# Optimization experiments

Measured on AMD Instinct MI355X. Metric: run time of the kernel, lower is better.

The kernel has to match this reference:

```python
import jax, jax.numpy as jnp
import numpy as np

E = 3_200_000
D = 16
N = 100_000


def setup_inputs() -> dict:
    key = jax.random.key(0)
    k1, k2 = jax.random.split(key)
    x = jax.random.normal(k1, (E, D), dtype=jnp.float32)
    edge_dst = jax.random.randint(k2, (E,), 0, N, dtype=jnp.int64)
    return {"x": x, "edge_dst": edge_dst, "num_nodes": N}


def reference(x, edge_dst, num_nodes):
    # sum_over_neighbours: scatter-add edge features to destination atoms -> [N, D]
    summed = jax.ops.segment_sum(x, edge_dst, num_segments=num_nodes)
    # number_of_neighbours(include_central_atom=True): per-atom edge count + 1
    counts = jax.ops.segment_sum(
        jnp.ones((x.shape[0],), dtype=x.dtype), edge_dst, num_segments=num_nodes
    ) + jnp.asarray(1.0, dtype=x.dtype)
    # left_aligned_div by sqrt(counts): broadcast counts over trailing feature dims
    return summed / jnp.sqrt(counts)[:, None]
```

## Files before the change

### kernel.cpp

```cpp
#include <hip/hip_runtime.h>

#define DFEAT 16
#define NPB 64
#define NPB_SHIFT 6
#define EB 8192
#define EB_SHIFT 13
#define BIN_THREADS 1024
#define SCAN_BLOCKS 256
#define SCAN_THREADS 256
#define SORT_CAP 4096

__global__ void na_bin_kernel(const int* __restrict__ edge_dst,
                              unsigned short* __restrict__ rank,
                              int* __restrict__ hist,
                              int E, int B, int nblocks) {
    extern __shared__ int h[];
    const int b = blockIdx.x;
    const int t = threadIdx.x;
    for (int i = t; i < B; i += BIN_THREADS) h[i] = 0;
    __syncthreads();
    const int base = b * EB;
    #pragma unroll
    for (int j = 0; j < EB / BIN_THREADS; ++j) {
        int e = base + j * BIN_THREADS + t;
        if (e < E) {
            int k = edge_dst[e] >> NPB_SHIFT;
            int r = atomicAdd(&h[k], 1);
            rank[e] = (unsigned short)r;
        }
    }
    __syncthreads();
    for (int i = t; i < B; i += BIN_THREADS)
        hist[(size_t)i * nblocks + b] = h[i];
}

__global__ void na_scan_partials(const int* __restrict__ data,
                                 int* __restrict__ blockSums, int M) {
    __shared__ int lds[SCAN_THREADS];
    const int b = blockIdx.x, t = threadIdx.x;
    const int chb = (M + SCAN_BLOCKS - 1) / SCAN_BLOCKS;
    const int bbeg = b * chb;
    const int bend = min(bbeg + chb, M);
    const int cht = (chb + SCAN_THREADS - 1) / SCAN_THREADS;
    const int beg = min(bbeg + t * cht, bend);
    const int end = min(beg + cht, bend);
    int s = 0;
    for (int i = beg; i < end; ++i) s += data[i];
    lds[t] = s;
    __syncthreads();
    for (int off = SCAN_THREADS / 2; off > 0; off >>= 1) {
        if (t < off) lds[t] += lds[t + off];
        __syncthreads();
    }
    if (t == 0) blockSums[b] = lds[0];
}

__global__ void na_scan_blocksums(const int* __restrict__ blockSums,
                                  int* __restrict__ blockOffs) {
    __shared__ int lds[SCAN_BLOCKS];
    const int t = threadIdx.x;
    int v = blockSums[t];
    lds[t] = v;
    __syncthreads();
    for (int off = 1; off < SCAN_BLOCKS; off <<= 1) {
        int add = (t >= off) ? lds[t - off] : 0;
        __syncthreads();
        lds[t] += add;
        __syncthreads();
    }
    blockOffs[t] = lds[t] - v;
}

__global__ void na_scan_final(int* __restrict__ data,
                              const int* __restrict__ blockOffs, int M) {
    __shared__ int lds[SCAN_THREADS];
    const int b = blockIdx.x, t = threadIdx.x;
    const int chb = (M + SCAN_BLOCKS - 1) / SCAN_BLOCKS;
    const int bbeg = b * chb;
    const int bend = min(bbeg + chb, M);
    const int cht = (chb + SCAN_THREADS - 1) / SCAN_THREADS;
    const int beg = min(bbeg + t * cht, bend);
    const int end = min(beg + cht, bend);
    int s = 0;
    for (int i = beg; i < end; ++i) s += data[i];
    lds[t] = s;
    __syncthreads();
    for (int off = 1; off < SCAN_THREADS; off <<= 1) {
        int add = (t >= off) ? lds[t - off] : 0;
        __syncthreads();
        lds[t] += add;
        __syncthreads();
    }
    int run = blockOffs[b] + lds[t] - s;
    for (int i = beg; i < end; ++i) {
        int c = data[i];
        data[i] = run;
        run += c;
    }
}

__global__ void na_scatter_bin(const int* __restrict__ edge_dst,
                               const unsigned short* __restrict__ rank,
                               const int* __restrict__ offs,
                               int* __restrict__ binned,
                               int E, int nblocks) {
    int e = blockIdx.x * blockDim.x + threadIdx.x;
    if (e >= E) return;
    int n = edge_dst[e];
    int k = n >> NPB_SHIFT;
    int b = e >> EB_SHIFT;
    int pos = offs[(size_t)k * nblocks + b] + (int)rank[e];
    binned[pos] = ((n & (NPB - 1)) << 22) | e;
}

__global__ void na_bucket_sort(int* __restrict__ binned,
                               const int* __restrict__ offs,
                               int* __restrict__ offsets,
                               int E, int N, int B, int nblocks) {
    __shared__ int buf[SORT_CAP];
    __shared__ int cnt[NPB];
    __shared__ int cur[NPB];
    __shared__ int excl[NPB + 1];
    const int k = blockIdx.x;
    const int t = threadIdx.x;

    const int beg = offs[(size_t)k * nblocks];
    const int end = (k + 1 < B) ? offs[(size_t)(k + 1) * nblocks] : E;
    const int sz = end - beg;

    if (t < NPB) { cnt[t] = 0; cur[t] = 0; }
    __syncthreads();

    for (int j = t; j < sz; j += 256) {
        int v = binned[beg + j];
        buf[j] = v;
        atomicAdd(&cnt[v >> 22], 1);
    }
    __syncthreads();

    if (t == 0) {
        int run = 0;
        for (int d = 0; d < NPB; ++d) { excl[d] = run; run += cnt[d]; }
        excl[NPB] = run;
    }
    __syncthreads();

    if (t < NPB) {
        int g = k * NPB + t;
        if (g < N) offsets[g] = beg + excl[t];
    }
    if (k == B - 1 && t == 0) offsets[N] = E;

    for (int j = t; j < sz; j += 256) {
        int v = buf[j];
        int d = v >> 22;
        int r = atomicAdd(&cur[d], 1);
        binned[beg + excl[d] + r] = v & 0x3FFFFF;
    }
}

__global__ void na_gather_kernel(const float* __restrict__ x,
                                 const int* __restrict__ edge_list,
                                 const int* __restrict__ offsets,
                                 float* __restrict__ out,
                                 int N) {
    int tid = blockIdx.x * blockDim.x + threadIdx.x;
    int node = tid >> 4;
    int f = tid & 15;
    if (node >= N) return;

    int beg = offsets[node];
    int end = offsets[node + 1];

    float acc = 0.0f;
    int i = beg;
    for (; i + 8 <= end; i += 8) {
        int e0 = edge_list[i + 0], e1 = edge_list[i + 1];
        int e2 = edge_list[i + 2], e3 = edge_list[i + 3];
        int e4 = edge_list[i + 4], e5 = edge_list[i + 5];
        int e6 = edge_list[i + 6], e7 = edge_list[i + 7];
        float v0 = x[(size_t)e0 * DFEAT + f];
        float v1 = x[(size_t)e1 * DFEAT + f];
        float v2 = x[(size_t)e2 * DFEAT + f];
        float v3 = x[(size_t)e3 * DFEAT + f];
        float v4 = x[(size_t)e4 * DFEAT + f];
        float v5 = x[(size_t)e5 * DFEAT + f];
        float v6 = x[(size_t)e6 * DFEAT + f];
        float v7 = x[(size_t)e7 * DFEAT + f];
        acc += ((v0 + v1) + (v2 + v3)) + ((v4 + v5) + (v6 + v7));
    }
    for (; i < end; ++i) acc += x[(size_t)edge_list[i] * DFEAT + f];

    float scale = rsqrtf((float)(end - beg) + 1.0f);
    out[(size_t)node * DFEAT + f] = acc * scale;
}

extern "C" void kernel_launch(void* const* d_in, const int* in_sizes, int n_in,
                              void* d_out, int out_size, void* d_ws, size_t ws_size,
                              hipStream_t stream) {
    const float* x        = (const float*)d_in[0];
    const int*   edge_dst = (const int*)d_in[1];
    float*       out      = (float*)d_out;

    const int E = in_sizes[1];
    const int N = out_size / DFEAT;
    const int B = (N + NPB - 1) >> NPB_SHIFT;
    const int nblocks = (E + EB - 1) >> EB_SHIFT;
    const int M = B * nblocks;

    unsigned short* rank = (unsigned short*)d_ws;
    int* binned    = (int*)((char*)d_ws + (((size_t)E * 2 + 3) & ~(size_t)3));
    int* hist      = binned + E;
    int* offsets   = hist + M;
    int* blockSums = offsets + N + 1;
    int* blockOffs = blockSums + SCAN_BLOCKS;

    na_bin_kernel<<<nblocks, BIN_THREADS, B * sizeof(int), stream>>>(
        edge_dst, rank, hist, E, B, nblocks);
    na_scan_partials<<<SCAN_BLOCKS, SCAN_THREADS, 0, stream>>>(hist, blockSums, M);
    na_scan_blocksums<<<1, SCAN_BLOCKS, 0, stream>>>(blockSums, blockOffs);
    na_scan_final<<<SCAN_BLOCKS, SCAN_THREADS, 0, stream>>>(hist, blockOffs, M);
    na_scatter_bin<<<(E + 255) / 256, 256, 0, stream>>>(
        edge_dst, rank, hist, binned, E, nblocks);
    na_bucket_sort<<<B, 256, 0, stream>>>(binned, hist, offsets, E, N, B, nblocks);

    const int gthreads = N * 16;
    na_gather_kernel<<<(gthreads + 255) / 256, 256, 0, stream>>>(
        x, binned, offsets, out, N);
}
```

Before: 141.9 us.

## Fuse bucket sort with gather, keep sorted edges in LDS, use float4 loads

The per-bucket local sort and the per-node gather are merged into one kernel. Sorted edge indices stay in shared memory instead of being written back to global memory and re-read, and the separate offsets array is dropped. The gather now reads x as float4, with four edge-strided lanes per node combined by shuffles. This removes one launch and one round trip of the edge list through global memory. In exchange the doubled shared-memory footprint may lower occupancy, and a slow fallback path handles buckets larger than the sort capacity.

```diff
diff --git a/kernel.cpp b/kernel.cpp
--- a/kernel.cpp
+++ b/kernel.cpp
@@ -113,14 +113,18 @@
     binned[pos] = ((n & (NPB - 1)) << 22) | e;
 }
 
-__global__ void na_bucket_sort(int* __restrict__ binned,
-                               const int* __restrict__ offs,
-                               int* __restrict__ offsets,
-                               int E, int N, int B, int nblocks) {
+__global__ __launch_bounds__(256, 4)
+void na_sort_gather(const float* __restrict__ x,
+                    const int* __restrict__ binned,
+                    const int* __restrict__ offs,
+                    float* __restrict__ out,
+                    int E, int N, int B, int nblocks) {
     __shared__ int buf[SORT_CAP];
+    __shared__ int sorted[SORT_CAP];
     __shared__ int cnt[NPB];
     __shared__ int cur[NPB];
     __shared__ int excl[NPB + 1];
+
     const int k = blockIdx.x;
     const int t = threadIdx.x;
 
@@ -131,68 +135,89 @@
     if (t < NPB) { cnt[t] = 0; cur[t] = 0; }
     __syncthreads();
 
-    for (int j = t; j < sz; j += 256) {
-        int v = binned[beg + j];
-        buf[j] = v;
-        atomicAdd(&cnt[v >> 22], 1);
-    }
-    __syncthreads();
-
-    if (t == 0) {
-        int run = 0;
-        for (int d = 0; d < NPB; ++d) { excl[d] = run; run += cnt[d]; }
-        excl[NPB] = run;
-    }
-    __syncthreads();
-
-    if (t < NPB) {
-        int g = k * NPB + t;
-        if (g < N) offsets[g] = beg + excl[t];
-    }
-    if (k == B - 1 && t == 0) offsets[N] = E;
-
-    for (int j = t; j < sz; j += 256) {
-        int v = buf[j];
-        int d = v >> 22;
-        int r = atomicAdd(&cur[d], 1);
-        binned[beg + excl[d] + r] = v & 0x3FFFFF;
-    }
-}
-
-__global__ void na_gather_kernel(const float* __restrict__ x,
-                                 const int* __restrict__ edge_list,
-                                 const int* __restrict__ offsets,
-                                 float* __restrict__ out,
-                                 int N) {
-    int tid = blockIdx.x * blockDim.x + threadIdx.x;
-    int node = tid >> 4;
-    int f = tid & 15;
-    if (node >= N) return;
-
-    int beg = offsets[node];
-    int end = offsets[node + 1];
-
-    float acc = 0.0f;
-    int i = beg;
-    for (; i + 8 <= end; i += 8) {
-        int e0 = edge_list[i + 0], e1 = edge_list[i + 1];
-        int e2 = edge_list[i + 2], e3 = edge_list[i + 3];
-        int e4 = edge_list[i + 4], e5 = edge_list[i + 5];
-        int e6 = edge_list[i + 6], e7 = edge_list[i + 7];
-        float v0 = x[(size_t)e0 * DFEAT + f];
-        float v1 = x[(size_t)e1 * DFEAT + f];
-        float v2 = x[(size_t)e2 * DFEAT + f];
-        float v3 = x[(size_t)e3 * DFEAT + f];
-        float v4 = x[(size_t)e4 * DFEAT + f];
-        float v5 = x[(size_t)e5 * DFEAT + f];
-        float v6 = x[(size_t)e6 * DFEAT + f];
-        float v7 = x[(size_t)e7 * DFEAT + f];
-        acc += ((v0 + v1) + (v2 + v3)) + ((v4 + v5) + (v6 + v7));
-    }
-    for (; i < end; ++i) acc += x[(size_t)edge_list[i] * DFEAT + f];
-
-    float scale = rsqrtf((float)(end - beg) + 1.0f);
-    out[(size_t)node * DFEAT + f] = acc * scale;
+    if (sz <= SORT_CAP) {
+        for (int j = t; j < sz; j += 256) {
+            int v = binned[beg + j];
+            buf[j] = v;
+            atomicAdd(&cnt[v >> 22], 1);
+        }
+        __syncthreads();
+        if (t == 0) {
+            int run = 0;
+            for (int d = 0; d < NPB; ++d) { excl[d] = run; run += cnt[d]; }
+            excl[NPB] = run;
+        }
+        __syncthreads();
+        for (int j = t; j < sz; j += 256) {
+            int v = buf[j];
+            int d = v >> 22;
+            int r = atomicAdd(&cur[d], 1);
+            sorted[excl[d] + r] = v & 0x3FFFFF;
+        }
+        __syncthreads();
+
+        const int g = t >> 4;
+        const int lane16 = t & 15;
+        const int es = lane16 >> 2;
+        const int q = lane16 & 3;
+        const float4* x4 = reinterpret_cast<const float4*>(x);
+
+        for (int ln = g; ln < NPB; ln += 16) {
+            int n = k * NPB + ln;
+            if (n >= N) break;
+            int lbeg = excl[ln], lend = excl[ln + 1];
+            float ax = 0.f, ay = 0.f, az = 0.f, aw = 0.f;
+
+            int i = lbeg + es;
+            for (; i + 12 < lend; i += 16) {
+                int e0 = sorted[i];
+                int e1 = sorted[i + 4];
+                int e2 = sorted[i + 8];
+                int e3 = sorted[i + 12];
+                float4 v0 = x4[(size_t)e0 * 4 + q];
+                float4 v1 = x4[(size_t)e1 * 4 + q];
+                float4 v2 = x4[(size_t)e2 * 4 + q];
+                float4 v3 = x4[(size_t)e3 * 4 + q];
+                ax += (v0.x + v1.x) + (v2.x + v3.x);
+                ay += (v0.y + v1.y) + (v2.y + v3.y);
+                az += (v0.z + v1.z) + (v2.z + v3.z);
+                aw += (v0.w + v1.w) + (v2.w + v3.w);
+            }
+            for (; i < lend; i += 4) {
+                int e0 = sorted[i];
+                float4 v0 = x4[(size_t)e0 * 4 + q];
+                ax += v0.x; ay += v0.y; az += v0.z; aw += v0.w;
+            }
+
+            ax += __shfl_xor(ax, 4); ay += __shfl_xor(ay, 4);
+            az += __shfl_xor(az, 4); aw += __shfl_xor(aw, 4);
+            ax += __shfl_xor(ax, 8); ay += __shfl_xor(ay, 8);
+            az += __shfl_xor(az, 8); aw += __shfl_xor(aw, 8);
+
+            float s = rsqrtf((float)(lend - lbeg) + 1.0f);
+            if (es == 0) {
+                float4 r; r.x = ax * s; r.y = ay * s; r.z = az * s; r.w = aw * s;
+                reinterpret_cast<float4*>(out)[(size_t)n * 4 + q] = r;
+            }
+        }
+    } else {
+        const int g = t >> 4;
+        const int f = t & 15;
+        for (int ln = g; ln < NPB; ln += 16) {
+            int n = k * NPB + ln;
+            if (n >= N) break;
+            float acc = 0.0f;
+            int deg = 0;
+            for (int j = 0; j < sz; ++j) {
+                int v = binned[beg + j];
+                if ((v >> 22) == ln) {
+                    acc += x[(size_t)(v & 0x3FFFFF) * DFEAT + f];
+                    ++deg;
+                }
+            }
+            out[(size_t)n * DFEAT + f] = acc * rsqrtf((float)deg + 1.0f);
+        }
+    }
 }
 
 extern "C" void kernel_launch(void* const* d_in, const int* in_sizes, int n_in,
@@ -211,8 +236,7 @@
     unsigned short* rank = (unsigned short*)d_ws;
     int* binned    = (int*)((char*)d_ws + (((size_t)E * 2 + 3) & ~(size_t)3));
     int* hist      = binned + E;
-    int* offsets   = hist + M;
-    int* blockSums = offsets + N + 1;
+    int* blockSums = hist + M;
     int* blockOffs = blockSums + SCAN_BLOCKS;
 
     na_bin_kernel<<<nblocks, BIN_THREADS, B * sizeof(int), stream>>>(
@@ -222,9 +246,5 @@
     na_scan_final<<<SCAN_BLOCKS, SCAN_THREADS, 0, stream>>>(hist, blockOffs, M);
     na_scatter_bin<<<(E + 255) / 256, 256, 0, stream>>>(
         edge_dst, rank, hist, binned, E, nblocks);
-    na_bucket_sort<<<B, 256, 0, stream>>>(binned, hist, offsets, E, N, B, nblocks);
-
-    const int gthreads = N * 16;
-    na_gather_kernel<<<(gthreads + 255) / 256, 256, 0, stream>>>(
-        x, binned, offsets, out, N);
-}
+    na_sort_gather<<<B, 256, 0, stream>>>(x, binned, hist, out, E, N, B, nblocks);
+}
```

Result: faster. 125.5 us (-11.6%).
